# Optimization experiments

Hardware: AMD Instinct MI355X
Metric: run time of the kernel (lower is better)

Reference implementation:

```python
import jax, jax.numpy as jnp
import numpy as np
import math

T, HW, M, D, DK, H, SIGMA = 16, 1024, 256, 768, 768, 8, 0.5
HD = DK // H
VHD = D // H
EPS = 1e-6
SCALE = 1.0 / math.sqrt(HD)


def _ln(x, g):
    # LayerNorm(eps=1e-6, bias=False)
    m = x.mean(-1, keepdims=True)
    v = ((x - m) ** 2).mean(-1, keepdims=True)
    return (x - m) / jnp.sqrt(v + EPS) * g


def setup_inputs() -> dict:
    key = jax.random.key(0)
    ks = jax.random.split(key, 16)
    s = 0.02
    features = jax.random.normal(ks[0], (T, HW, D), jnp.float32)
    tracks = jax.random.uniform(ks[1], (T, M, 2), jnp.float32)
    track_pos_embeddings = jax.random.normal(ks[2], (T, M, D), jnp.float32)
    feature_pos_embeddings = jax.random.normal(ks[3], (T, HW, D), jnp.float32)
    g = jnp.linspace(0.0, 1.0, 32)
    feature_positions = jnp.stack(jnp.meshgrid(g, g, indexing='ij'), axis=-1).reshape(HW, 2)
    return {
        'features': features,
        'tracks': tracks,
        'feature_positions': feature_positions,
        'track_pos_embeddings': track_pos_embeddings,
        'feature_pos_embeddings': feature_pos_embeddings,
        # AttentionalSampling params (nn.Linear weights are [out,in])
        'Wq_s': jax.random.normal(ks[4], (DK, D)) * s,
        'Wk_s': jax.random.normal(ks[5], (DK, D)) * s,
        'Wv_s': jax.random.normal(ks[6], (D, D)) * s,
        'qg_s': jnp.ones((DK,), jnp.float32),
        'kg_s': jnp.ones((DK,), jnp.float32),
        'Wo_s': jax.random.normal(ks[7], (D, D)) * s,
        # AttentionalSplatting params
        'Wq_p': jax.random.normal(ks[8], (DK, D)) * s,
        'Wk_p': jax.random.normal(ks[9], (DK, D)) * s,
        'Wv_p': jax.random.normal(ks[10], (D, D)) * s,
        'qg_p': jnp.ones((DK,), jnp.float32),
        'kg_p': jnp.ones((DK,), jnp.float32),
        'Wout_p': jax.random.normal(ks[11], (D, D)) * s,
    }


def reference(features, tracks, feature_positions, track_pos_embeddings,
              feature_pos_embeddings, Wq_s, Wk_s, Wv_s, qg_s, kg_s, Wo_s,
              Wq_p, Wk_p, Wv_p, qg_p, kg_p, Wout_p):
    # per-frame Gaussian spatial bias from squared euclidean distances
    # d2[t,m,n] = ||tracks[t,m] - feature_positions[n]||^2  -> [T, M, HW]
    d2 = ((tracks[:, :, None, :] - feature_positions[None, None, :, :]) ** 2).sum(-1)
    bias = -d2 / (2.0 * SIGMA ** 2)  # [T, M, HW]

    # ---- Attentional Sampling: tracks query features ----
    Q = _ln(track_pos_embeddings @ Wq_s.T, qg_s)          # [T, M, DK]
    K = _ln((features + feature_pos_embeddings) @ Wk_s.T, kg_s)  # [T, HW, DK]
    V = features @ Wv_s.T                                  # [T, HW, D]
    Qh = Q.reshape(T, M, H, HD).transpose(0, 2, 1, 3)      # [T, H, M, HD]
    Kh = K.reshape(T, HW, H, HD).transpose(0, 2, 1, 3)     # [T, H, HW, HD]
    Vh = V.reshape(T, HW, H, VHD).transpose(0, 2, 1, 3)    # [T, H, HW, VHD]
    scores = jnp.einsum('thmd,thnd->thmn', Qh, Kh) * SCALE + bias[:, None]
    A = jax.nn.softmax(scores, axis=-1)
    sampled = jnp.einsum('thmn,thnd->thmd', A, Vh)
    sampled = sampled.transpose(0, 2, 1, 3).reshape(T, M, D) @ Wo_s.T  # [T, M, D]

    # ---- Attentional Splatting: features query tracks ----
    Q2 = _ln(feature_pos_embeddings @ Wq_p.T, qg_p)        # [T, HW, DK]
    K2 = _ln(track_pos_embeddings @ Wk_p.T, kg_p)          # [T, M, DK]
    V2 = sampled @ Wv_p.T                                   # [T, M, D]
    Q2h = Q2.reshape(T, HW, H, HD).transpose(0, 2, 1, 3)   # [T, H, HW, HD]
    K2h = K2.reshape(T, M, H, HD).transpose(0, 2, 1, 3)    # [T, H, M, HD]
    V2h = V2.reshape(T, M, H, VHD).transpose(0, 2, 1, 3)   # [T, H, M, VHD]
    bias_t = jnp.swapaxes(bias, 1, 2)                       # [T, HW, M] (cdist is symmetric)
    scores2 = jnp.einsum('thnd,thmd->thnm', Q2h, K2h) * SCALE + bias_t[:, None]
    A2 = jax.nn.softmax(scores2, axis=-1)
    upd = jnp.einsum('thnm,thmd->thnd', A2, V2h)
    feature_updates = upd.transpose(0, 2, 1, 3).reshape(T, HW, D) @ Wout_p.T
    return features + feature_updates
```

## Files before the change

kernel.cpp:

```cpp
#include <hip/hip_runtime.h>

#define DD 768
#define HDIM 96
#define ATT_SCALE 0.10206207261596575f

typedef float floatx4 __attribute__((ext_vector_type(4)));
typedef __bf16 bf16;
typedef bf16 bf16x8 __attribute__((ext_vector_type(8)));
typedef bf16 bf16x4 __attribute__((ext_vector_type(4)));
typedef bf16 bf16x2 __attribute__((ext_vector_type(2)));

__device__ __forceinline__ void gl2lds16(const bf16* g, bf16* l) {
  __builtin_amdgcn_global_load_lds(
      (const __attribute__((address_space(1))) void*)g,
      (__attribute__((address_space(3))) void*)l, 16, 0, 0);
}

__global__ __launch_bounds__(256) void prep(
    const float* __restrict__ features, const float* __restrict__ fpe,
    const float* __restrict__ tpe,
    const float* w0, const float* w1, const float* w2, const float* w3,
    const float* w4, const float* w5, const float* w6, const float* w7,
    bf16* __restrict__ Fb, bf16* __restrict__ Xb, bf16* __restrict__ Feb,
    bf16* __restrict__ Tb, bf16* __restrict__ Wb, bf16* __restrict__ WoT) {
  const int b = blockIdx.x;
  const int tid = threadIdx.x;
  if (b < 3072) {
    const int i = (b * 256 + tid) * 16;
    floatx4 f[4], e[4];
#pragma unroll
    for (int k = 0; k < 4; k++) f[k] = *(const floatx4*)(features + i + k * 4);
#pragma unroll
    for (int k = 0; k < 4; k++) e[k] = *(const floatx4*)(fpe + i + k * 4);
    bf16 fv[16], xv[16], ev[16];
#pragma unroll
    for (int k = 0; k < 16; k++) {
      float ff = f[k >> 2][k & 3], ee = e[k >> 2][k & 3];
      fv[k] = (bf16)ff; ev[k] = (bf16)ee; xv[k] = (bf16)(ff + ee);
    }
    *(bf16x8*)(Fb + i) = *(bf16x8*)&fv[0];
    *(bf16x8*)(Fb + i + 8) = *(bf16x8*)&fv[8];
    *(bf16x8*)(Xb + i) = *(bf16x8*)&xv[0];
    *(bf16x8*)(Xb + i + 8) = *(bf16x8*)&xv[8];
    *(bf16x8*)(Feb + i) = *(bf16x8*)&ev[0];
    *(bf16x8*)(Feb + i + 8) = *(bf16x8*)&ev[8];
  } else if (b < 3840) {
    const int i = ((b - 3072) * 256 + tid) * 16;
    floatx4 s[4];
#pragma unroll
    for (int k = 0; k < 4; k++) s[k] = *(const floatx4*)(tpe + i + k * 4);
    bf16 v[16];
#pragma unroll
    for (int k = 0; k < 16; k++) v[k] = (bf16)s[k >> 2][k & 3];
    *(bf16x8*)(Tb + i) = *(bf16x8*)&v[0];
    *(bf16x8*)(Tb + i + 8) = *(bf16x8*)&v[8];
  } else if (b < 4992) {
    const int sub = b - 3840;
    const int wi = sub / 144, xb = sub % 144;
    const float* srcs[8] = {w0, w1, w2, w3, w4, w5, w6, w7};
    const float* s = srcs[wi];
    bf16* d = Wb + (size_t)wi * 589824;
    const int i = (xb * 256 + tid) * 16;
    floatx4 sv[4];
#pragma unroll
    for (int k = 0; k < 4; k++) sv[k] = *(const floatx4*)(s + i + k * 4);
    bf16 v[16];
#pragma unroll
    for (int k = 0; k < 16; k++) v[k] = (bf16)sv[k >> 2][k & 3];
    *(bf16x8*)(d + i) = *(bf16x8*)&v[0];
    *(bf16x8*)(d + i + 8) = *(bf16x8*)&v[8];
  } else {
    __shared__ float Ts[64][65];
    const int sub = b - 4992;
    const int X0 = (sub % 12) * 64, Y0 = (sub / 12) * 64;
    const int r = tid >> 2;
    const int c4 = (tid & 3) * 16;
    const float* src = w3 + (size_t)(Y0 + r) * DD + X0 + c4;
#pragma unroll
    for (int k = 0; k < 16; k += 4) {
      floatx4 v = *(const floatx4*)(src + k);
      Ts[r][c4 + k] = v[0]; Ts[r][c4 + k + 1] = v[1];
      Ts[r][c4 + k + 2] = v[2]; Ts[r][c4 + k + 3] = v[3];
    }
    __syncthreads();
    bf16 o[16];
#pragma unroll
    for (int k = 0; k < 16; k++) o[k] = (bf16)Ts[c4 + k][r];
    *(bf16x8*)(WoT + (size_t)(X0 + r) * DD + Y0 + c4) = *(bf16x8*)&o[0];
    *(bf16x8*)(WoT + (size_t)(X0 + r) * DD + Y0 + c4 + 8) = *(bf16x8*)&o[8];
  }
}

__device__ __forceinline__ void ln_row(bf16* x, const float* g, int lane) {
  float v[12], s = 0.f, ss = 0.f;
#pragma unroll
  for (int j = 0; j < 3; j++) {
    bf16x4 b = *(const bf16x4*)&x[j * 256 + lane * 4];
#pragma unroll
    for (int e = 0; e < 4; e++) {
      float t = (float)b[e];
      v[j * 4 + e] = t; s += t; ss += t * t;
    }
  }
#pragma unroll
  for (int o = 32; o > 0; o >>= 1) { s += __shfl_xor(s, o); ss += __shfl_xor(ss, o); }
  const float mean = s * (1.0f / DD);
  const float inv = rsqrtf(ss * (1.0f / DD) - mean * mean + 1e-6f);
#pragma unroll
  for (int j = 0; j < 3; j++) {
    floatx4 gg = *(const floatx4*)&g[j * 256 + lane * 4];
    bf16x4 o4;
#pragma unroll
    for (int e = 0; e < 4; e++) o4[e] = (bf16)((v[j * 4 + e] - mean) * inv * gg[e]);
    *(bf16x4*)&x[j * 256 + lane * 4] = o4;
  }
}

__global__ __launch_bounds__(256) void ln_all(bf16* X0, const float* g0,
                                              bf16* X1, const float* g1,
                                              bf16* X2, const float* g2,
                                              bf16* X3, const float* g3) {
  const int b = blockIdx.x;
  bf16* X; const float* g; int base;
  if (b < 4096)      { X = X0; g = g0; base = b; }
  else if (b < 8192) { X = X1; g = g1; base = b - 4096; }
  else if (b < 9216) { X = X2; g = g2; base = b - 8192; }
  else               { X = X3; g = g3; base = b - 9216; }
  const int w = threadIdx.x >> 6, lane = threadIdx.x & 63;
  ln_row(X + (size_t)(base * 4 + w) * DD, g, lane);
}

#define BAR() do { __builtin_amdgcn_sched_barrier(0); \
                   __builtin_amdgcn_s_barrier(); \
                   __builtin_amdgcn_sched_barrier(0); } while (0)
#define VMW(n) asm volatile("s_waitcnt vmcnt(" #n ")" ::: "memory")
#define LGKM0() do { asm volatile("s_waitcnt lgkmcnt(0)" ::: "memory"); \
                     __builtin_amdgcn_sched_barrier(0); } while (0)

template <int MODE>
__device__ __forceinline__ void gemm256(const bf16* __restrict__ A,
                                        const bf16* __restrict__ W,
                                        bf16* __restrict__ Cb,
                                        float* __restrict__ Cf,
                                        const float* __restrict__ addsrc,
                                        bf16* lds, int row0, int col0) {
  const int tid = threadIdx.x;
  const int lane = tid & 63;
  const int w = tid >> 6;
  const int wm = (w & 1) * 128;
  const int wn = (w >> 1) * 64;
  const int fr = lane & 15;
  const int quad = lane >> 4;
  const int f7 = fr & 7;

  const int srow = tid >> 3;
  const int sswz = ((tid & 7) ^ (srow & 7)) * 8;
  const bf16* Ag = A + (size_t)(row0 + srow) * DD + sswz;
  const bf16* Wg = W + (size_t)(col0 + srow) * DD + sswz;
  bf16* dA = lds + tid * 8;
  bf16* dB = lds + 32768 + tid * 8;

#define STGA(tau, h) do { \
    gl2lds16(Ag + (size_t)((h) * 128) * DD + (tau) * 64, \
             dA + ((tau) & 1) * 16384 + (h) * 8192); \
    gl2lds16(Ag + (size_t)((h) * 128 + 64) * DD + (tau) * 64, \
             dA + ((tau) & 1) * 16384 + (h) * 8192 + 4096); \
  } while (0)
#define STGB(tau, h) do { \
    gl2lds16(Wg + (size_t)((h) * 128) * DD + (tau) * 64, \
             dB + ((tau) & 1) * 16384 + (h) * 8192); \
    gl2lds16(Wg + (size_t)((h) * 128 + 64) * DD + (tau) * 64, \
             dB + ((tau) & 1) * 16384 + (h) * 8192 + 4096); \
  } while (0)

  const int sl0 = (quad ^ f7) * 8;
  const int sl1 = ((4 | quad) ^ f7) * 8;

#define LDA8(buf, mh) do { \
    _Pragma("unroll") for (int m = 0; m < 4; m++) { \
      const bf16* p = lds + (buf) * 16384 + (wm + (mh) * 64 + m * 16 + fr) * 64; \
      af[m][0] = *(const bf16x8*)(p + sl0); \
      af[m][1] = *(const bf16x8*)(p + sl1); } \
  } while (0)
#define LDB4(buf, nh, dst) do { \
    _Pragma("unroll") for (int n = 0; n < 2; n++) { \
      const bf16* p = lds + 32768 + (buf) * 16384 + (wn + (nh) * 32 + n * 16 + fr) * 64; \
      dst[n][0] = *(const bf16x8*)(p + sl0); \
      dst[n][1] = *(const bf16x8*)(p + sl1); } \
  } while (0)
#define MM16(mh, nbase, bb) do { \
    __builtin_amdgcn_s_setprio(1); \
    _Pragma("unroll") for (int m = 0; m < 4; m++) \
    _Pragma("unroll") for (int n = 0; n < 2; n++) { \
      acc[(mh) * 4 + m][(nbase) + n] = __builtin_amdgcn_mfma_f32_16x16x32_bf16( \
          af[m][0], bb[n][0], acc[(mh) * 4 + m][(nbase) + n], 0, 0, 0); \
      acc[(mh) * 4 + m][(nbase) + n] = __builtin_amdgcn_mfma_f32_16x16x32_bf16( \
          af[m][1], bb[n][1], acc[(mh) * 4 + m][(nbase) + n], 0, 0, 0); } \
    __builtin_amdgcn_s_setprio(0); \
  } while (0)

  floatx4 acc[8][4];

  STGB(0, 0); STGB(0, 1); STGA(0, 0); STGA(0, 1);
  STGB(1, 0); STGB(1, 1);
#pragma unroll
  for (int i = 0; i < 8; i++)
#pragma unroll
    for (int j = 0; j < 4; j++) acc[i][j] = (floatx4){0, 0, 0, 0};
  VMW(4);
  BAR();

  bf16x8 af[4][2], b0[2][2], b1[2][2];

  for (int it = 0; it < 6; ++it) {
    const int a = 2 * it;
    const bool stg = (it < 5);
    LDA8(0, 0); LDB4(0, 0, b0);
    STGA(a + 1, 0);
    BAR();
    MM16(0, 0, b0);
    BAR();
    LDB4(0, 1, b1);
    STGA(a + 1, 1);
    BAR();
    MM16(0, 2, b1);
    BAR();
    LDA8(0, 1);
    if (stg) STGB(a + 2, 0);
    BAR();
    MM16(1, 2, b1);
    BAR();
    if (stg) STGB(a + 2, 1);
    BAR();
    MM16(1, 0, b0);
    if (stg) { VMW(4); } else { VMW(0); }
    BAR();
    LDA8(1, 0); LDB4(1, 0, b0);
    if (stg) STGA(a + 2, 0);
    BAR();
    MM16(0, 0, b0);
    BAR();
    LDB4(1, 1, b1);
    if (stg) STGA(a + 2, 1);
    BAR();
    MM16(0, 2, b1);
    BAR();
    LDA8(1, 1);
    if (stg) STGB(a + 3, 0);
    BAR();
    MM16(1, 2, b1);
    BAR();
    if (stg) STGB(a + 3, 1);
    BAR();
    MM16(1, 0, b0);
    if (stg) VMW(4);
    BAR();
  }

  float* sc = (float*)lds + (size_t)w * (16 * 68);
  const int er = lane >> 2;
  const int ec = lane & 3;
#pragma unroll
  for (int m = 0; m < 8; m++) {
    const int grow = row0 + wm + m * 16 + er;
    const int gcol = col0 + wn + ec * 16;
    floatx4 av[4];
    if (MODE == 1) {
      const float* as = addsrc + (size_t)grow * DD + gcol;
#pragma unroll
      for (int c = 0; c < 4; c++) av[c] = *(const floatx4*)(as + c * 4);
    }
#pragma unroll
    for (int n = 0; n < 4; n++)
#pragma unroll
      for (int r = 0; r < 4; r++)
        sc[(quad * 4 + r) * 68 + n * 16 + fr] = acc[m][n][r];
    LGKM0();
    floatx4 rv[4];
#pragma unroll
    for (int c = 0; c < 4; c++) rv[c] = *(const floatx4*)&sc[er * 68 + ec * 16 + c * 4];
    LGKM0();
    if (MODE == 0) {
      bf16x8 o0, o1;
#pragma unroll
      for (int e = 0; e < 8; e++) {
        o0[e] = (bf16)rv[e >> 2][e & 3];
        o1[e] = (bf16)rv[2 + (e >> 2)][e & 3];
      }
      *(bf16x8*)(Cb + (size_t)grow * DD + gcol) = o0;
      *(bf16x8*)(Cb + (size_t)grow * DD + gcol + 8) = o1;
    } else {
      float* cp = Cf + (size_t)grow * DD + gcol;
#pragma unroll
      for (int c = 0; c < 4; c++)
        *(floatx4*)(cp + c * 4) = rv[c] + av[c];
    }
  }
#undef STGA
#undef STGB
#undef LDA8
#undef LDB4
#undef MM16
}

__global__ __launch_bounds__(512, 2) void gemm_all(
    const bf16* Xb, const bf16* Fb, const bf16* Feb, const bf16* Tb,
    const bf16* Wb, const bf16* WoT,
    bf16* Kc, bf16* Vc, bf16* Qb2, bf16* Qc, bf16* K2, bf16* Wcr) {
  __shared__ bf16 lds[65536];
  const size_t SW = (size_t)768 * 768;
  const int z = blockIdx.z;
  if (z == 0)
    gemm256<0>(Xb, Wb + 1 * SW, Kc, nullptr, nullptr, lds,
               blockIdx.x * 256, blockIdx.y * 256);
  else if (z == 1)
    gemm256<0>(Fb, Wb + 2 * SW, Vc, nullptr, nullptr, lds,
               blockIdx.x * 256, blockIdx.y * 256);
  else if (z == 2)
    gemm256<0>(Feb, Wb + 4 * SW, Qb2, nullptr, nullptr, lds,
               blockIdx.x * 256, blockIdx.y * 256);
  else {
    const int x = blockIdx.x;
    if (x < 16)
      gemm256<0>(Tb, Wb + 0 * SW, Qc, nullptr, nullptr, lds,
                 x * 256, blockIdx.y * 256);
    else if (x < 32)
      gemm256<0>(Tb, Wb + 5 * SW, K2, nullptr, nullptr, lds,
                 (x - 16) * 256, blockIdx.y * 256);
    else if (x < 35)
      gemm256<0>(Wb + 6 * SW, WoT, Wcr, nullptr, nullptr, lds,
                 (x - 32) * 256, blockIdx.y * 256);
  }
}

__global__ __launch_bounds__(512, 2) void gemm_b(const bf16* A, const bf16* W, bf16* C) {
  __shared__ bf16 lds[65536];
  gemm256<0>(A, W, C, nullptr, nullptr, lds, blockIdx.x * 256, blockIdx.y * 256);
}

__global__ __launch_bounds__(512, 2) void gemm_final(const bf16* A, const bf16* W,
                                                     float* C, const float* addsrc) {
  __shared__ bf16 lds[65536];
  gemm256<1>(A, W, nullptr, C, addsrc, lds, blockIdx.x * 256, blockIdx.y * 256);
}

template <int SPLIT>
__global__ __launch_bounds__(512, 4) void attn512(
    const bf16* __restrict__ Qb, const bf16* __restrict__ Kb,
    const bf16* __restrict__ Vb, bf16* __restrict__ Ob,
    float* __restrict__ Ml,
    const float* __restrict__ qpos, int qpos_ts,
    const float* __restrict__ kpos, int kpos_ts,
    int nq, int nk, int npq, int nsp) {
  const int b = blockIdx.x;
  const int h = b & 7;
  const int t = (b >> 3) & 15;
  const int rest = b >> 7;
  const int qt = rest % npq;
  const int sp = rest / npq;
  const int klen = nk / nsp;
  const int k0s = sp * klen;
  const int q0 = qt * 128;
  const bf16* Q = Qb + (size_t)t * nq * DD + h * HDIM;
  const bf16* K = Kb + (size_t)t * nk * DD + h * HDIM;
  const bf16* V = Vb + (size_t)t * nk * DD + h * HDIM;
  bf16* O = Ob + (size_t)(SPLIT ? (sp * 16 + t) : t) * nq * DD + h * HDIM;
  const float* qp = qpos + (size_t)t * qpos_ts;
  const float* kp = kpos + (size_t)t * kpos_ts;

  __shared__ bf16 Ks[64 * 104];
  __shared__ bf16 Vt[96 * 72];
  __shared__ bf16 Ps[2 * 64 * 72];
  __shared__ float Kpl[512];

  const int tid = threadIdx.x;
  const int w = tid >> 6;
  const int g = w >> 2;
  const int wl = w & 3;
  const int lane = tid & 63;
  const int fr = lane & 15;
  const int quad = lane >> 4;
  const int rowb = wl * 16;
  const int qgb = q0 + g * 64;
  bf16* Pg = &Ps[g * 64 * 72];

  bf16x8 qf[3];
  {
    const bf16* qrow = Q + (size_t)(qgb + rowb + fr) * DD;
#pragma unroll
    for (int c = 0; c < 3; c++) qf[c] = *(const bf16x8*)(qrow + c * 32 + quad * 8);
  }
  float qx[4], qy[4];
#pragma unroll
  for (int r = 0; r < 4; r++) {
    int qi = qgb + rowb + quad * 4 + r;
    qx[r] = qp[qi * 2];
    qy[r] = qp[qi * 2 + 1];
  }

  float lrow[4] = {0.f, 0.f, 0.f, 0.f};
  floatx4 oacc[6];
#pragma unroll
  for (int d = 0; d < 6; d++) oacc[d] = (floatx4){0, 0, 0, 0};

  const int krA = tid >> 3, kcA = (tid & 7) * 8;
  const int krB = (tid & 255) >> 2, kcB = 64 + (tid & 3) * 8;
  const int nb = (tid & 31) * 2, db = (tid >> 5) * 6;

  Kpl[tid] = kp[(size_t)k0s * 2 + tid];

  struct VR { unsigned a, b, c; };
  bf16x8 kaA, kbA, kaB, kbB;
  VR vA0, vA1, vB0, vB1;

  auto loadreg = [&](int n0, bf16x8& ka, bf16x8& kb, VR& r0, VR& r1) {
    ka = *(const bf16x8*)(K + (size_t)(n0 + krA) * DD + kcA);
    if (tid < 256) kb = *(const bf16x8*)(K + (size_t)(n0 + krB) * DD + kcB);
    const unsigned* g0 = (const unsigned*)(V + (size_t)(n0 + nb) * DD + db);
    const unsigned* g1 = (const unsigned*)(V + (size_t)(n0 + nb + 1) * DD + db);
    r0.a = g0[0]; r0.b = g0[1]; r0.c = g0[2];
    r1.a = g1[0]; r1.b = g1[1]; r1.c = g1[2];
  };
  auto writelds = [&](const bf16x8& ka, const bf16x8& kb, const VR& r0, const VR& r1) {
    *(bf16x8*)&Ks[krA * 104 + kcA] = ka;
    if (tid < 256) *(bf16x8*)&Ks[krB * 104 + kcB] = kb;
    bf16 t0[6], t1[6];
    *(unsigned*)&t0[0] = r0.a; *(unsigned*)&t0[2] = r0.b; *(unsigned*)&t0[4] = r0.c;
    *(unsigned*)&t1[0] = r1.a; *(unsigned*)&t1[2] = r1.b; *(unsigned*)&t1[4] = r1.c;
#pragma unroll
    for (int dd = 0; dd < 6; dd++) {
      bf16x2 v2 = {t0[dd], t1[dd]};
      *(bf16x2*)&Vt[(db + dd) * 72 + nb] = v2;
    }
  };
  auto compute = [&](int rel) {
    floatx4 s4[4];
#pragma unroll
    for (int j = 0; j < 4; j++) {
      floatx4 sa = {0, 0, 0, 0};
#pragma unroll
      for (int c = 0; c < 3; c++) {
        bf16x8 kf = *(const bf16x8*)&Ks[(j * 16 + fr) * 104 + c * 32 + quad * 8];
        sa = __builtin_amdgcn_mfma_f32_16x16x32_bf16(qf[c], kf, sa, 0, 0, 0);
      }
      s4[j] = sa;
    }
    float kxx[4], kyy[4];
#pragma unroll
    for (int j = 0; j < 4; j++) {
      int ki = (rel + j * 16 + fr) * 2;
      kxx[j] = Kpl[ki];
      kyy[j] = Kpl[ki + 1];
    }
#pragma unroll
    for (int j = 0; j < 4; j++)
#pragma unroll
      for (int r = 0; r < 4; r++) {
        float dx = qx[r] - kxx[j], dy = qy[r] - kyy[j];
        float sv = s4[j][r] * ATT_SCALE - 2.0f * (dx * dx + dy * dy);
        float pv = __expf(sv);
        lrow[r] += pv;
        Pg[(rowb + quad * 4 + r) * 72 + j * 16 + fr] = (bf16)pv;
      }
    bf16x8 pf0 = *(const bf16x8*)&Pg[(rowb + fr) * 72 + quad * 8];
    bf16x8 pf1 = *(const bf16x8*)&Pg[(rowb + fr) * 72 + 32 + quad * 8];
#pragma unroll
    for (int d = 0; d < 6; d++) {
      bf16x8 v0 = *(const bf16x8*)&Vt[(d * 16 + fr) * 72 + quad * 8];
      bf16x8 v1 = *(const bf16x8*)&Vt[(d * 16 + fr) * 72 + 32 + quad * 8];
      oacc[d] = __builtin_amdgcn_mfma_f32_16x16x32_bf16(pf0, v0, oacc[d], 0, 0, 0);
      oacc[d] = __builtin_amdgcn_mfma_f32_16x16x32_bf16(pf1, v1, oacc[d], 0, 0, 0);
    }
  };

  const int NT = klen >> 6;
  loadreg(k0s, kaA, kbA, vA0, vA1);
  for (int n = 0; n < NT; n += 2) {
    __syncthreads();
    writelds(kaA, kbA, vA0, vA1);
    if (n + 1 < NT) loadreg(k0s + (n + 1) * 64, kaB, kbB, vB0, vB1);
    __syncthreads();
    compute(n * 64);
    if (n + 1 >= NT) break;
    __syncthreads();
    writelds(kaB, kbB, vB0, vB1);
    if (n + 2 < NT) loadreg(k0s + (n + 2) * 64, kaA, kbA, vA0, vA1);
    __syncthreads();
    compute((n + 1) * 64);
  }

#pragma unroll
  for (int r = 0; r < 4; r++)
#pragma unroll
    for (int o = 1; o < 16; o <<= 1) lrow[r] += __shfl_xor(lrow[r], o);

#pragma unroll
  for (int r = 0; r < 4; r++) {
    int row = qgb + rowb + quad * 4 + r;
    if (SPLIT) {
#pragma unroll
      for (int d = 0; d < 6; d++)
        O[(size_t)row * DD + d * 16 + fr] = (bf16)oacc[d][r];
      if (fr == 0)
        Ml[((size_t)(sp * 16 + t) * 8 + h) * nq + row] = lrow[r];
    } else {
      float inv = 1.0f / lrow[r];
#pragma unroll
      for (int d = 0; d < 6; d++)
        O[(size_t)row * DD + d * 16 + fr] = (bf16)(oacc[d][r] * inv);
    }
  }
}

__global__ __launch_bounds__(256) void combine4(const bf16* __restrict__ Op,
                                                const float* __restrict__ Ml,
                                                bf16* __restrict__ Out) {
  const int row = blockIdx.x;
  const int t = row >> 8;
  const int q = row & 255;
  __shared__ float Mls[32];
  const int tid = threadIdx.x;
  if (tid < 32) {
    int s = tid >> 3, hh = tid & 7;
    Mls[tid] = Ml[((size_t)(s * 16 + t) * 8 + hh) * 256 + q];
  }
  __syncthreads();
  if (tid < 192) {
    const int dim = tid * 4;
    const int hh = dim / 96;
    float o[4] = {0.f, 0.f, 0.f, 0.f};
    float lsum = 0.f;
#pragma unroll
    for (int s = 0; s < 4; s++) {
      lsum += Mls[s * 8 + hh];
      bf16x4 v = *(const bf16x4*)&Op[((size_t)(s * 16 + t) * 256 + q) * DD + dim];
#pragma unroll
      for (int e = 0; e < 4; e++) o[e] += (float)v[e];
    }
    const float inv = 1.0f / lsum;
    bf16x4 ov;
#pragma unroll
    for (int e = 0; e < 4; e++) ov[e] = (bf16)(o[e] * inv);
    *(bf16x4*)&Out[(size_t)row * DD + dim] = ov;
  }
}

extern "C" void kernel_launch(void* const* d_in, const int* in_sizes, int n_in,
                              void* d_out, int out_size, void* d_ws, size_t ws_size,
                              hipStream_t stream) {
  const float* features = (const float*)d_in[0];
  const float* tracks   = (const float*)d_in[1];
  const float* fpos     = (const float*)d_in[2];
  const float* tpe      = (const float*)d_in[3];
  const float* fpe      = (const float*)d_in[4];
  const float* Wq_s     = (const float*)d_in[5];
  const float* Wk_s     = (const float*)d_in[6];
  const float* Wv_s     = (const float*)d_in[7];
  const float* qg_s     = (const float*)d_in[8];
  const float* kg_s     = (const float*)d_in[9];
  const float* Wo_s     = (const float*)d_in[10];
  const float* Wq_p     = (const float*)d_in[11];
  const float* Wk_p     = (const float*)d_in[12];
  const float* Wv_p     = (const float*)d_in[13];
  const float* qg_p     = (const float*)d_in[14];
  const float* kg_p     = (const float*)d_in[15];
  const float* Wout_p   = (const float*)d_in[16];
  float* out = (float*)d_out;

  const size_t SB = (size_t)16 * 1024 * 768;
  const size_t SS = (size_t)16 * 256 * 768;
  const size_t SW = (size_t)768 * 768;
  bf16* p = (bf16*)d_ws;
  bf16* Fb  = p; p += SB;
  bf16* Xb  = p; p += SB;
  bf16* Feb = p; p += SB;
  bf16* Kc  = p; p += SB;
  bf16* Vc  = p; p += SB;
  bf16* Qb2 = p; p += SB;
  bf16* Tb  = p; p += SS;
  bf16* Qc  = p; p += SS;
  bf16* K2  = p; p += SS;
  bf16* Sh  = p; p += SS;
  bf16* Op  = p; p += 4 * SS;
  bf16* Wb  = p; p += 8 * SW;
  bf16* WoT = p; p += SW;
  bf16* Wcr = p; p += SW;
  float* Ml = (float*)p;
  bf16* V2 = Qc; bf16* U = Fb;

  dim3 blk(256);

  prep<<<5136, blk, 0, stream>>>(features, fpe, tpe,
                                 Wq_s, Wk_s, Wv_s, Wo_s, Wq_p, Wk_p, Wv_p, Wout_p,
                                 Fb, Xb, Feb, Tb, Wb, WoT);
  gemm_all<<<dim3(64, 3, 4), dim3(512), 0, stream>>>(Xb, Fb, Feb, Tb, Wb, WoT,
                                                     Kc, Vc, Qb2, Qc, K2, Wcr);
  ln_all<<<10240, blk, 0, stream>>>(Kc, kg_s, Qb2, qg_p, Qc, qg_s, K2, kg_p);
  attn512<1><<<1024, dim3(512), 0, stream>>>(Qc, Kc, Vc, Op, Ml,
                                             tracks, 512, fpos, 0, 256, 1024, 2, 4);
  combine4<<<4096, blk, 0, stream>>>(Op, Ml, Sh);
  gemm_b<<<dim3(16, 3), dim3(512), 0, stream>>>(Sh, Wcr, V2);
  attn512<0><<<1024, dim3(512), 0, stream>>>(Qb2, K2, V2, U, nullptr,
                                             fpos, 0, tracks, 512, 1024, 256, 8, 1);
  gemm_final<<<dim3(64, 3), dim3(512), 0, stream>>>(U, Wb + 7 * SW, out, features);
}
```

Measured before the change: 444.0 us.

## Halve sampling-attention KV split and use smaller-tile GEMM for V2 projection

The first attention pass now splits the 1024 keys into 2 chunks instead of 4, which halves the grid, and the combine kernel merges 2 partials instead of 4. The Kpl buffer is enlarged and loaded in a loop so it can hold the longer key chunk. The small M=4096 GEMM that produces V2 switches from 256x256 tiles on 48 blocks to a new 128x128 tile kernel on 192 blocks of 256 threads, to fill more CUs. The trade is fewer attention blocks and less combine traffic against more serial work per attention block.

```diff
diff --git a/kernel.cpp b/kernel.cpp
--- a/kernel.cpp
+++ b/kernel.cpp
@@ -301,6 +301,72 @@
 #undef LDA8
 #undef LDB4
 #undef MM16
+}
+
+__device__ __forceinline__ void gemm_core64(const bf16* __restrict__ A,
+                                            const bf16* __restrict__ W,
+                                            bf16* __restrict__ Cb,
+                                            bf16* As, bf16* Ws,
+                                            int row0, int col0) {
+  const int tid = threadIdx.x;
+  const int lane = tid & 63;
+  const int w = tid >> 6;
+  const int wm = (w & 1) * 64;
+  const int wn = (w >> 1) * 64;
+  const int fr = lane & 15;
+  const int quad = lane >> 4;
+  const int srow = tid >> 2;
+  const int scol = (tid & 3) * 8;
+  const bf16* Ag = A + (size_t)(row0 + srow) * DD + scol;
+  const bf16* Wg = W + (size_t)(col0 + srow) * DD + scol;
+  bf16* AsD = &As[tid * 8];
+  bf16* WsD = &Ws[tid * 8];
+
+  floatx4 acc[4][4];
+#pragma unroll
+  for (int i = 0; i < 4; i++)
+#pragma unroll
+    for (int j = 0; j < 4; j++) acc[i][j] = (floatx4){0, 0, 0, 0};
+
+  for (int k0 = 0; k0 < DD; k0 += 64) {
+    __syncthreads();
+    gl2lds16(Ag + k0, AsD);
+    gl2lds16(Ag + k0 + (size_t)64 * DD, AsD + 2048);
+    gl2lds16(Wg + k0, WsD);
+    gl2lds16(Wg + k0 + (size_t)64 * DD, WsD + 2048);
+    gl2lds16(Ag + k0 + 32, AsD + 4096);
+    gl2lds16(Ag + k0 + 32 + (size_t)64 * DD, AsD + 4096 + 2048);
+    gl2lds16(Wg + k0 + 32, WsD + 4096);
+    gl2lds16(Wg + k0 + 32 + (size_t)64 * DD, WsD + 4096 + 2048);
+    __syncthreads();
+#pragma unroll
+    for (int half = 0; half < 2; half++) {
+      const bf16* Ah = As + half * 4096;
+      const bf16* Wh = Ws + half * 4096;
+      bf16x8 af[4], bfr[4];
+#pragma unroll
+      for (int i = 0; i < 4; i++)
+        af[i] = *(const bf16x8*)&Ah[(wm + i * 16 + fr) * 32 + quad * 8];
+#pragma unroll
+      for (int j = 0; j < 4; j++)
+        bfr[j] = *(const bf16x8*)&Wh[(wn + j * 16 + fr) * 32 + quad * 8];
+#pragma unroll
+      for (int i = 0; i < 4; i++)
+#pragma unroll
+        for (int j = 0; j < 4; j++)
+          acc[i][j] = __builtin_amdgcn_mfma_f32_16x16x32_bf16(af[i], bfr[j], acc[i][j], 0, 0, 0);
+    }
+  }
+#pragma unroll
+  for (int i = 0; i < 4; i++)
+#pragma unroll
+    for (int j = 0; j < 4; j++)
+#pragma unroll
+      for (int r = 0; r < 4; r++) {
+        const int row = row0 + wm + i * 16 + quad * 4 + r;
+        const int col = col0 + wn + j * 16 + fr;
+        Cb[(size_t)row * DD + col] = (bf16)acc[i][j][r];
+      }
 }
 
 __global__ __launch_bounds__(512, 2) void gemm_all(
@@ -333,9 +399,9 @@
   }
 }
 
-__global__ __launch_bounds__(512, 2) void gemm_b(const bf16* A, const bf16* W, bf16* C) {
-  __shared__ bf16 lds[65536];
-  gemm256<0>(A, W, C, nullptr, nullptr, lds, blockIdx.x * 256, blockIdx.y * 256);
+__global__ __launch_bounds__(256) void gemm_b(const bf16* A, const bf16* W, bf16* C) {
+  __shared__ bf16 As[8192], Ws[8192];
+  gemm_core64(A, W, C, As, Ws, blockIdx.x * 128, blockIdx.y * 128);
 }
 
 __global__ __launch_bounds__(512, 2) void gemm_final(const bf16* A, const bf16* W,
@@ -371,7 +437,7 @@
   __shared__ bf16 Ks[64 * 104];
   __shared__ bf16 Vt[96 * 72];
   __shared__ bf16 Ps[2 * 64 * 72];
-  __shared__ float Kpl[512];
+  __shared__ float Kpl[1024];
 
   const int tid = threadIdx.x;
   const int w = tid >> 6;
@@ -407,7 +473,7 @@
   const int krB = (tid & 255) >> 2, kcB = 64 + (tid & 3) * 8;
   const int nb = (tid & 31) * 2, db = (tid >> 5) * 6;
 
-  Kpl[tid] = kp[(size_t)k0s * 2 + tid];
+  for (int i = tid; i < klen * 2; i += 512) Kpl[i] = kp[(size_t)k0s * 2 + i];
 
   struct VR { unsigned a, b, c; };
   bf16x8 kaA, kbA, kaB, kbB;
@@ -512,15 +578,15 @@
   }
 }
 
-__global__ __launch_bounds__(256) void combine4(const bf16* __restrict__ Op,
+__global__ __launch_bounds__(256) void combine2(const bf16* __restrict__ Op,
                                                 const float* __restrict__ Ml,
                                                 bf16* __restrict__ Out) {
   const int row = blockIdx.x;
   const int t = row >> 8;
   const int q = row & 255;
-  __shared__ float Mls[32];
+  __shared__ float Mls[16];
   const int tid = threadIdx.x;
-  if (tid < 32) {
+  if (tid < 16) {
     int s = tid >> 3, hh = tid & 7;
     Mls[tid] = Ml[((size_t)(s * 16 + t) * 8 + hh) * 256 + q];
   }
@@ -531,7 +597,7 @@
     float o[4] = {0.f, 0.f, 0.f, 0.f};
     float lsum = 0.f;
 #pragma unroll
-    for (int s = 0; s < 4; s++) {
+    for (int s = 0; s < 2; s++) {
       lsum += Mls[s * 8 + hh];
       bf16x4 v = *(const bf16x4*)&Op[((size_t)(s * 16 + t) * 256 + q) * DD + dim];
 #pragma unroll
@@ -596,10 +662,10 @@
   gemm_all<<<dim3(64, 3, 4), dim3(512), 0, stream>>>(Xb, Fb, Feb, Tb, Wb, WoT,
                                                      Kc, Vc, Qb2, Qc, K2, Wcr);
   ln_all<<<10240, blk, 0, stream>>>(Kc, kg_s, Qb2, qg_p, Qc, qg_s, K2, kg_p);
-  attn512<1><<<1024, dim3(512), 0, stream>>>(Qc, Kc, Vc, Op, Ml,
-                                             tracks, 512, fpos, 0, 256, 1024, 2, 4);
-  combine4<<<4096, blk, 0, stream>>>(Op, Ml, Sh);
-  gemm_b<<<dim3(16, 3), dim3(512), 0, stream>>>(Sh, Wcr, V2);
+  attn512<1><<<512, dim3(512), 0, stream>>>(Qc, Kc, Vc, Op, Ml,
+                                            tracks, 512, fpos, 0, 256, 1024, 2, 2);
+  combine2<<<4096, blk, 0, stream>>>(Op, Ml, Sh);
+  gemm_b<<<dim3(32, 6), blk, 0, stream>>>(Sh, Wcr, V2);
   attn512<0><<<1024, dim3(512), 0, stream>>>(Qb2, K2, V2, U, nullptr,
                                              fpos, 0, tracks, 512, 1024, 256, 8, 1);
   gemm_final<<<dim3(64, 3), dim3(512), 0, stream>>>(U, Wb + 7 * SW, out, features);
```

Result: no change. 438.5 us (-1.2%).
